# Kernel optimization log

Measured on AMD Instinct MI355X. Metric: run time of the kernel, lower is better.

## Reference

```python
import jax, jax.numpy as jnp
import numpy as np

D = 2048      # hidden dim
H = 16        # heads
BSZ = 4       # batch
L = 2048      # seq len
BASE_DT = 0.1


def setup_inputs() -> dict:
    key = jax.random.key(0)
    ks = jax.random.split(key, 9)
    s = 1.0 / np.sqrt(D)
    x = jax.random.normal(ks[0], (BSZ, L, D), dtype=jnp.float32)
    v = jax.random.normal(ks[1], (BSZ, L, D), dtype=jnp.float32)
    force = jax.random.normal(ks[2], (BSZ, L, D), dtype=jnp.float32)
    WA = jax.random.normal(ks[3], (D, D), dtype=jnp.float32) * s
    bA = jnp.zeros((D,), dtype=jnp.float32)
    WB = jax.random.normal(ks[4], (D, D), dtype=jnp.float32) * s
    bB = jnp.zeros((D,), dtype=jnp.float32)
    Wdt = jax.random.normal(ks[5], (D, D), dtype=jnp.float32) * s
    bdt = jnp.zeros((D,), dtype=jnp.float32)
    # base_dt_scales buffer: 1.5**head_index, repeated head_dim times
    scales = jnp.repeat(1.5 ** jnp.arange(H, dtype=jnp.float32), D // H)
    return {"x": x, "v": v, "force": force, "WA": WA, "bA": bA,
            "WB": WB, "bB": bB, "Wdt": Wdt, "bdt": bdt, "scales": scales}


def _combine(e1, e2):
    # associative op for v_t = a_t * v_{t-1} + b_t ; e1 is the earlier element
    a1, b1 = e1
    a2, b2 = e2
    return a1 * a2, a2 * b1 + b2


def reference(x, v, force, WA, bA, WB, bB, Wdt, bdt, scales):
    # x is LayerNorm-ed in the original but the result is unused; v is unused.
    A = jax.nn.sigmoid(force @ WA + bA)                      # [B, L, D] in (0,1)
    dt = jax.nn.softplus(force @ Wdt + bdt) * BASE_DT * scales  # per-head dt scaling
    B_val = (force @ WB + bB) * dt
    # parallel associative scan over the sequence axis: v_t = A_t v_{t-1} + B_t
    _, v_seq = jax.lax.associative_scan(_combine, (A, B_val), axis=1)
    # second scan has A=1 -> plain prefix sum
    x_seq = jnp.cumsum(v_seq * dt, axis=1)
    return x_seq, v_seq
```

## Files before the change

### kernel.cpp

```cpp
#include <hip/hip_runtime.h>
#include <hip/hip_bf16.h>
#include <cstdint>
#include <cstddef>

#define D_DIM 2048
#define L_SEQ 2048
#define B_SZ 4
#define M_ROWS (B_SZ * L_SEQ)
#define NT_COLS (3 * D_DIM)
#define NCH 16
#define CHUNK (L_SEQ / NCH)

typedef __bf16 bf16_t;
typedef bf16_t bf16x4 __attribute__((ext_vector_type(4)));
typedef bf16_t bf16x8 __attribute__((ext_vector_type(8)));
typedef float f32x4 __attribute__((ext_vector_type(4)));

__device__ __forceinline__ void gl_lds16(const void* g, void* l) {
    __builtin_amdgcn_global_load_lds(
        (const __attribute__((address_space(1))) unsigned int*)g,
        (__attribute__((address_space(3))) unsigned int*)l, 16, 0, 0);
}

__global__ __launch_bounds__(256) void cvt_bf16_kernel(
    const float* __restrict__ in, bf16_t* __restrict__ out, int n4)
{
    int i = blockIdx.x * 256 + threadIdx.x;
    if (i >= n4) return;
    float4 f = ((const float4*)in)[i];
    bf16x4 o;
    o[0] = (bf16_t)f.x; o[1] = (bf16_t)f.y; o[2] = (bf16_t)f.z; o[3] = (bf16_t)f.w;
    ((bf16x4*)out)[i] = o;
}

__global__ __launch_bounds__(256) void transpose_w_kernel(
    const float* __restrict__ W, bf16_t* __restrict__ Wt)
{
    __shared__ float tile[32][33];
    int j0 = blockIdx.x * 32, k0 = blockIdx.y * 32;
    int tx = threadIdx.x, ty = threadIdx.y;
#pragma unroll
    for (int i = 0; i < 4; i++) {
        int k = k0 + ty + i * 8;
        tile[ty + i * 8][tx] = W[(size_t)k * D_DIM + j0 + tx];
    }
    __syncthreads();
#pragma unroll
    for (int i = 0; i < 4; i++) {
        int j = j0 + ty + i * 8;
        Wt[(size_t)j * D_DIM + k0 + tx] = (bf16_t)tile[tx][ty + i * 8];
    }
}

__global__ __launch_bounds__(256) void gemm_fused_kernel(
    const bf16_t* __restrict__ Abf,
    const bf16_t* __restrict__ Wt,
    const float* __restrict__ bA, const float* __restrict__ bdt,
    const float* __restrict__ bB, const float* __restrict__ scales,
    float* __restrict__ outA,
    float* __restrict__ outDT,
    float* __restrict__ outB)
{
    __shared__ bf16_t lds_a[128 * 32];
    __shared__ bf16_t lds_b[128 * 32];

    const int bm0 = blockIdx.x * 128;
    const int bn0 = blockIdx.y * 128;
    const int t = threadIdx.x;
    const int lane = t & 63, w = t >> 6;
    const int wr = (w >> 1) * 64;
    const int wc = (w & 1) * 64;

    f32x4 acc[4][4] = {};

    const int lin0 = t, lin1 = t + 256;
    const int ar0 = lin0 >> 2, ac0 = (lin0 & 3) * 8;
    const int ar1 = lin1 >> 2, ac1 = (lin1 & 3) * 8;
    const int frow = lane & 15;
    const int fk = (lane >> 4) * 8;

    for (int k0 = 0; k0 < D_DIM; k0 += 32) {
        gl_lds16(Abf + (size_t)(bm0 + ar0) * D_DIM + k0 + ac0, lds_a + w * 512);
        gl_lds16(Abf + (size_t)(bm0 + ar1) * D_DIM + k0 + ac1, lds_a + 2048 + w * 512);
        gl_lds16(Wt  + (size_t)(bn0 + ar0) * D_DIM + k0 + ac0, lds_b + w * 512);
        gl_lds16(Wt  + (size_t)(bn0 + ar1) * D_DIM + k0 + ac1, lds_b + 2048 + w * 512);
        __syncthreads();

        bf16x8 af[4], bfr[4];
#pragma unroll
        for (int m = 0; m < 4; m++)
            af[m] = *(const bf16x8*)&lds_a[(wr + m * 16 + frow) * 32 + fk];
#pragma unroll
        for (int n = 0; n < 4; n++)
            bfr[n] = *(const bf16x8*)&lds_b[(wc + n * 16 + frow) * 32 + fk];
#pragma unroll
        for (int m = 0; m < 4; m++)
#pragma unroll
            for (int n = 0; n < 4; n++)
                acc[m][n] = __builtin_amdgcn_mfma_f32_16x16x32_bf16(
                    af[m], bfr[n], acc[m][n], 0, 0, 0);
        __syncthreads();
    }

    const int seg = bn0 >> 11;
    const int dbase = (bn0 & 2047) + wc + (lane & 15);
    const int rowbase = bm0 + wr + ((lane >> 4) << 2);
#pragma unroll
    for (int m = 0; m < 4; m++) {
#pragma unroll
        for (int n = 0; n < 4; n++) {
            int d = dbase + n * 16;
#pragma unroll
            for (int r = 0; r < 4; r++) {
                int gm = rowbase + m * 16 + r;
                size_t idx = (size_t)gm * D_DIM + d;
                float val = acc[m][n][r];
                if (seg == 0) {
                    outA[idx] = 1.0f / (1.0f + __expf(-(val + bA[d])));
                } else if (seg == 1) {
                    float xx = val + bdt[d];
                    float sp = xx > 0.f ? xx + log1pf(__expf(-xx)) : log1pf(__expf(xx));
                    outDT[idx] = sp * 0.1f * scales[d];
                } else {
                    outB[idx] = val + bB[d];
                }
            }
        }
    }
}

__global__ __launch_bounds__(256) void scan_pass1_kernel(
    const float* __restrict__ Aarr, const float* __restrict__ Braw,
    const float* __restrict__ dtarr, float4* __restrict__ agg)
{
    int tid = blockIdx.x * 256 + threadIdx.x;
    int d = tid & (D_DIM - 1);
    int c = (tid >> 11) & (NCH - 1);
    int b = tid >> 15;
    size_t base = ((size_t)b * L_SEQ + c * CHUNK) * D_DIM + d;
    float P = 1.f, R = 0.f, U = 0.f, Wg = 0.f;
#pragma unroll 4
    for (int tt = 0; tt < CHUNK; tt++) {
        size_t idx = base + (size_t)tt * D_DIM;
        float a = Aarr[idx], rb = Braw[idx], dt = dtarr[idx];
        float bv = rb * dt;
        float da = dt * a;
        R = da * P + R;
        Wg = da * U + dt * bv + Wg;
        U = a * U + bv;
        P = a * P;
    }
    agg[tid] = make_float4(P, R, U, Wg);
}

__global__ __launch_bounds__(256) void scan_pass2_kernel(
    const float4* __restrict__ agg, float2* __restrict__ pre)
{
    int tid = blockIdx.x * 256 + threadIdx.x;
    int d = tid & (D_DIM - 1);
    int b = tid >> 11;
    float v = 0.f, x = 0.f;
#pragma unroll
    for (int c = 0; c < NCH; c++) {
        int i = ((b * NCH + c) << 11) + d;
        float4 g = agg[i];
        pre[i] = make_float2(v, x);
        float vn = g.x * v + g.z;
        x = g.y * v + x + g.w;
        v = vn;
    }
}

__global__ __launch_bounds__(256) void scan_pass3_kernel(
    const float* __restrict__ dtarr, const float2* __restrict__ pre,
    float* __restrict__ xout ,
    float* __restrict__ vout )
{
    int tid = blockIdx.x * 256 + threadIdx.x;
    int d = tid & (D_DIM - 1);
    int c = (tid >> 11) & (NCH - 1);
    int b = tid >> 15;
    float2 s = pre[((b * NCH + c) << 11) + d];
    float v = s.x, x = s.y;
    size_t base = ((size_t)b * L_SEQ + c * CHUNK) * D_DIM + d;
#pragma unroll 4
    for (int tt = 0; tt < CHUNK; tt++) {
        size_t idx = base + (size_t)tt * D_DIM;
        float a = xout[idx];
        float rb = vout[idx];
        float dt = dtarr[idx];
        v = a * v + rb * dt;
        x = x + v * dt;
        vout[idx] = v;
        xout[idx] = x;
    }
}

extern "C" void kernel_launch(void* const* d_in, const int* in_sizes, int n_in,
                              void* d_out, int out_size, void* d_ws, size_t ws_size,
                              hipStream_t stream) {
    const float* force  = (const float*)d_in[2];
    const float* WA     = (const float*)d_in[3];
    const float* bA     = (const float*)d_in[4];
    const float* WB     = (const float*)d_in[5];
    const float* bB     = (const float*)d_in[6];
    const float* Wdt    = (const float*)d_in[7];
    const float* bdt    = (const float*)d_in[8];
    const float* scales = (const float*)d_in[9];

    float* xout = (float*)d_out;
    float* vout = xout + (size_t)M_ROWS * D_DIM;

    char* ws = (char*)d_ws;
    bf16_t* fbf = (bf16_t*)ws;
    bf16_t* wt  = (bf16_t*)(ws + (size_t)33554432);
    float*  dtv = (float*)(ws + (size_t)33554432 + 25165824);
    float4* agg = (float4*)(ws + (size_t)33554432 + 25165824 + 67108864);
    float2* pre = (float2*)(ws + (size_t)33554432 + 25165824 + 67108864 + 2097152);

    {
        int n4 = M_ROWS * D_DIM / 4;
        cvt_bf16_kernel<<<n4 / 256, 256, 0, stream>>>(force, fbf, n4);
    }
    {
        dim3 grid(D_DIM / 32, D_DIM / 32), block(32, 8);
        transpose_w_kernel<<<grid, block, 0, stream>>>(WA,  wt);
        transpose_w_kernel<<<grid, block, 0, stream>>>(Wdt, wt + (size_t)D_DIM * D_DIM);
        transpose_w_kernel<<<grid, block, 0, stream>>>(WB,  wt + (size_t)2 * D_DIM * D_DIM);
    }
    {
        dim3 grid(M_ROWS / 128, NT_COLS / 128);
        gemm_fused_kernel<<<grid, 256, 0, stream>>>(fbf, wt, bA, bdt, bB, scales,
                                                    xout, dtv, vout);
    }
    scan_pass1_kernel<<<(B_SZ * NCH * D_DIM) / 256, 256, 0, stream>>>(xout, vout, dtv, agg);
    scan_pass2_kernel<<<(B_SZ * D_DIM) / 256, 256, 0, stream>>>(agg, pre);
    scan_pass3_kernel<<<(B_SZ * NCH * D_DIM) / 256, 256, 0, stream>>>(dtv, pre, xout, vout);
}
```

Measured before the change: 498.6 us.

## Rewrite GEMM as 256x256 tile, 8-wave, double-buffered LDS pipeline with swizzle

Replaces the 128x128, single-buffered GEMM with a 256x256-tile kernel using 8 waves, a 128KB double-buffered LDS staging area filled asynchronously through global_load_lds, and XOR-swizzled LDS addressing. Loads for the next k-tiles are interleaved with MFMA groups using explicit vmcnt waits, raw barriers and setprio. Block IDs are remapped for better L2 locality. Bias loads are hoisted out of the epilogue. The aim is to raise MFMA utilization and cut per-k-step barrier stalls and LDS bank conflicts, at the cost of high register pressure and fragile manual synchronization.

After: 709.4 us. +42.3%, slower.

```diff
diff --git a/kernel.cpp b/kernel.cpp
--- a/kernel.cpp
+++ b/kernel.cpp
@@ -10,6 +10,7 @@
 #define NT_COLS (3 * D_DIM)
 #define NCH 16
 #define CHUNK (L_SEQ / NCH)
+#define KTILES (D_DIM / 64)
 
 typedef __bf16 bf16_t;
 typedef bf16_t bf16x4 __attribute__((ext_vector_type(4)));
@@ -21,6 +22,10 @@
         (const __attribute__((address_space(1))) unsigned int*)g,
         (__attribute__((address_space(3))) unsigned int*)l, 16, 0, 0);
 }
+
+#define BAR() asm volatile("s_barrier" ::: "memory")
+#define VMCNT4() asm volatile("s_waitcnt vmcnt(4)" ::: "memory")
+#define VMCNT0() asm volatile("s_waitcnt vmcnt(0)" ::: "memory")
 
 __global__ __launch_bounds__(256) void cvt_bf16_kernel(
     const float* __restrict__ in, bf16_t* __restrict__ out, int n4)
@@ -52,7 +57,39 @@
     }
 }
 
-__global__ __launch_bounds__(256) void gemm_fused_kernel(
+__device__ __forceinline__ void stage_half(const bf16_t* gp, int kofs,
+                                           char* ldsreg, int w, int lane)
+{
+    const int r0 = w * 32 + (lane >> 2);
+    const int gc = (((lane & 3) ^ ((lane >> 3) & 3)) << 3);
+    gl_lds16(gp + (size_t)r0 * D_DIM + kofs + gc, ldsreg + w * 2048);
+    gl_lds16(gp + (size_t)(r0 + 16) * D_DIM + kofs + gc, ldsreg + w * 2048 + 1024);
+}
+
+#define READ_FRAGS(BUF, KS, AF, BF) {                                          \
+    const char* ra_ = lds + (BUF) * 32768 + (KS) * 16384;                      \
+    const char* rb_ = ra_ + 65536;                                             \
+    _Pragma("unroll") for (int mm = 0; mm < 4; mm++)                           \
+        AF[mm] = *(const bf16x8*)(ra_ + ((wmBase + mm * 16) << 6) + loff);     \
+    _Pragma("unroll") for (int nn = 0; nn < 4; nn++)                           \
+        BF[nn] = *(const bf16x8*)(rb_ + ((wnBase + nn * 16) << 6) + loff);     \
+    _Pragma("unroll") for (int mm = 4; mm < 8; mm++)                           \
+        AF[mm] = *(const bf16x8*)(ra_ + ((wmBase + mm * 16) << 6) + loff); }
+
+#define MFMA_QUAD(MH, AF, BF)                                                  \
+    __builtin_amdgcn_s_setprio(1);                                             \
+    _Pragma("unroll") for (int mm = 0; mm < 4; mm++)                           \
+        _Pragma("unroll") for (int nn = 0; nn < 4; nn++)                       \
+            acc[(MH) * 4 + mm][nn] = __builtin_amdgcn_mfma_f32_16x16x32_bf16(  \
+                AF[(MH) * 4 + mm], BF[nn], acc[(MH) * 4 + mm][nn], 0, 0, 0);   \
+    __builtin_amdgcn_s_setprio(0);
+
+#define STAGE_A(BUF, T, KS) stage_half(gA, (T) * 64 + (KS) * 32,               \
+        lds + (BUF) * 32768 + (KS) * 16384, w, lane)
+#define STAGE_B(BUF, T, KS) stage_half(gB, (T) * 64 + (KS) * 32,               \
+        lds + 65536 + (BUF) * 32768 + (KS) * 16384, w, lane)
+
+__global__ __launch_bounds__(512, 2) void gemm_fused_kernel(
     const bf16_t* __restrict__ Abf,
     const bf16_t* __restrict__ Wt,
     const float* __restrict__ bA, const float* __restrict__ bdt,
@@ -61,71 +98,124 @@
     float* __restrict__ outDT,
     float* __restrict__ outB)
 {
-    __shared__ bf16_t lds_a[128 * 32];
-    __shared__ bf16_t lds_b[128 * 32];
-
-    const int bm0 = blockIdx.x * 128;
-    const int bn0 = blockIdx.y * 128;
-    const int t = threadIdx.x;
-    const int lane = t & 63, w = t >> 6;
-    const int wr = (w >> 1) * 64;
-    const int wc = (w & 1) * 64;
-
-    f32x4 acc[4][4] = {};
-
-    const int lin0 = t, lin1 = t + 256;
-    const int ar0 = lin0 >> 2, ac0 = (lin0 & 3) * 8;
-    const int ar1 = lin1 >> 2, ac1 = (lin1 & 3) * 8;
+    __shared__ __align__(1024) char lds[131072];
+
+    const int bid = blockIdx.x;
+    const int u = (bid & 7) * 96 + (bid >> 3);
+    const int bm0 = (u / 24) * 256;
+    const int bn0 = (u % 24) * 256;
+
+    const int tid = threadIdx.x;
+    const int lane = tid & 63;
+    const int w = tid >> 6;
+    const int wm = w >> 2;
+    const int wn = w & 3;
+    const int wmBase = wm * 128;
+    const int wnBase = wn * 64;
+
     const int frow = lane & 15;
-    const int fk = (lane >> 4) * 8;
-
-    for (int k0 = 0; k0 < D_DIM; k0 += 32) {
-        gl_lds16(Abf + (size_t)(bm0 + ar0) * D_DIM + k0 + ac0, lds_a + w * 512);
-        gl_lds16(Abf + (size_t)(bm0 + ar1) * D_DIM + k0 + ac1, lds_a + 2048 + w * 512);
-        gl_lds16(Wt  + (size_t)(bn0 + ar0) * D_DIM + k0 + ac0, lds_b + w * 512);
-        gl_lds16(Wt  + (size_t)(bn0 + ar1) * D_DIM + k0 + ac1, lds_b + 2048 + w * 512);
-        __syncthreads();
-
-        bf16x8 af[4], bfr[4];
-#pragma unroll
-        for (int m = 0; m < 4; m++)
-            af[m] = *(const bf16x8*)&lds_a[(wr + m * 16 + frow) * 32 + fk];
-#pragma unroll
-        for (int n = 0; n < 4; n++)
-            bfr[n] = *(const bf16x8*)&lds_b[(wc + n * 16 + frow) * 32 + fk];
-#pragma unroll
-        for (int m = 0; m < 4; m++)
+    const int loff = frow * 64 + (((lane >> 4) << 4) ^ (((frow >> 1) & 3) << 4));
+
+    const bf16_t* gA = Abf + (size_t)bm0 * D_DIM;
+    const bf16_t* gB = Wt + (size_t)bn0 * D_DIM;
+
+    f32x4 acc[8][4] = {};
+    bf16x8 af0[8], af1[8], bf0[4], bf1[4];
+
+    STAGE_A(0, 0, 0); STAGE_B(0, 0, 0); STAGE_A(0, 0, 1); STAGE_B(0, 0, 1);
+    STAGE_A(1, 1, 0); STAGE_B(1, 1, 0);
+    VMCNT4();
+    BAR();
+
+    for (int i = 0; i < KTILES / 2; ++i) {
+        const int t = 2 * i;
+        const bool nl = (i < KTILES / 2 - 1);
+
+        READ_FRAGS(0, 0, af0, bf0);
+        STAGE_A(1, t + 1, 1);
+        BAR();
+        MFMA_QUAD(0, af0, bf0);
+        BAR();
+        READ_FRAGS(0, 1, af1, bf1);
+        STAGE_B(1, t + 1, 1);
+        BAR();
+        MFMA_QUAD(1, af0, bf0);
+        BAR();
+        if (nl) STAGE_A(0, t + 2, 0);
+        BAR();
+        MFMA_QUAD(0, af1, bf1);
+        BAR();
+        if (nl) STAGE_B(0, t + 2, 0);
+        BAR();
+        MFMA_QUAD(1, af1, bf1);
+        if (nl) { VMCNT4(); } else { VMCNT0(); }
+        BAR();
+        READ_FRAGS(1, 0, af0, bf0);
+        if (nl) STAGE_A(0, t + 2, 1);
+        BAR();
+        MFMA_QUAD(0, af0, bf0);
+        BAR();
+        READ_FRAGS(1, 1, af1, bf1);
+        if (nl) STAGE_B(0, t + 2, 1);
+        BAR();
+        MFMA_QUAD(1, af0, bf0);
+        BAR();
+        if (nl) STAGE_A(1, t + 3, 0);
+        BAR();
+        MFMA_QUAD(0, af1, bf1);
+        BAR();
+        if (nl) STAGE_B(1, t + 3, 0);
+        BAR();
+        MFMA_QUAD(1, af1, bf1);
+        if (nl) { VMCNT4(); }
+        BAR();
+    }
+
+    const int seg = bn0 >> 11;
+    const int colb = (bn0 & 2047) + wnBase + (lane & 15);
+    const int rowb = bm0 + wmBase + ((lane >> 4) << 2);
+
+    if (seg == 0) {
+        float bias[4];
+#pragma unroll
+        for (int n = 0; n < 4; n++) bias[n] = bA[colb + n * 16];
+#pragma unroll
+        for (int m = 0; m < 8; m++)
 #pragma unroll
             for (int n = 0; n < 4; n++)
-                acc[m][n] = __builtin_amdgcn_mfma_f32_16x16x32_bf16(
-                    af[m], bfr[n], acc[m][n], 0, 0, 0);
-        __syncthreads();
-    }
-
-    const int seg = bn0 >> 11;
-    const int dbase = (bn0 & 2047) + wc + (lane & 15);
-    const int rowbase = bm0 + wr + ((lane >> 4) << 2);
-#pragma unroll
-    for (int m = 0; m < 4; m++) {
-#pragma unroll
-        for (int n = 0; n < 4; n++) {
-            int d = dbase + n * 16;
-#pragma unroll
-            for (int r = 0; r < 4; r++) {
-                int gm = rowbase + m * 16 + r;
-                size_t idx = (size_t)gm * D_DIM + d;
-                float val = acc[m][n][r];
-                if (seg == 0) {
-                    outA[idx] = 1.0f / (1.0f + __expf(-(val + bA[d])));
-                } else if (seg == 1) {
-                    float xx = val + bdt[d];
+#pragma unroll
+                for (int r = 0; r < 4; r++) {
+                    size_t idx = (size_t)(rowb + m * 16 + r) * D_DIM + colb + n * 16;
+                    outA[idx] = 1.0f / (1.0f + __expf(-(acc[m][n][r] + bias[n])));
+                }
+    } else if (seg == 1) {
+        float bias[4], sc[4];
+#pragma unroll
+        for (int n = 0; n < 4; n++) { bias[n] = bdt[colb + n * 16]; sc[n] = scales[colb + n * 16]; }
+#pragma unroll
+        for (int m = 0; m < 8; m++)
+#pragma unroll
+            for (int n = 0; n < 4; n++)
+#pragma unroll
+                for (int r = 0; r < 4; r++) {
+                    size_t idx = (size_t)(rowb + m * 16 + r) * D_DIM + colb + n * 16;
+                    float xx = acc[m][n][r] + bias[n];
                     float sp = xx > 0.f ? xx + log1pf(__expf(-xx)) : log1pf(__expf(xx));
-                    outDT[idx] = sp * 0.1f * scales[d];
-                } else {
-                    outB[idx] = val + bB[d];
+                    outDT[idx] = sp * 0.1f * sc[n];
                 }
-            }
-        }
+    } else {
+        float bias[4];
+#pragma unroll
+        for (int n = 0; n < 4; n++) bias[n] = bB[colb + n * 16];
+#pragma unroll
+        for (int m = 0; m < 8; m++)
+#pragma unroll
+            for (int n = 0; n < 4; n++)
+#pragma unroll
+                for (int r = 0; r < 4; r++) {
+                    size_t idx = (size_t)(rowb + m * 16 + r) * D_DIM + colb + n * 16;
+                    outB[idx] = acc[m][n][r] + bias[n];
+                }
     }
 }
 
@@ -173,8 +263,7 @@
 
 __global__ __launch_bounds__(256) void scan_pass3_kernel(
     const float* __restrict__ dtarr, const float2* __restrict__ pre,
-    float* __restrict__ xout ,
-    float* __restrict__ vout )
+    float* __restrict__ xout, float* __restrict__ vout)
 {
     int tid = blockIdx.x * 256 + threadIdx.x;
     int d = tid & (D_DIM - 1);
@@ -229,8 +318,8 @@
         transpose_w_kernel<<<grid, block, 0, stream>>>(WB,  wt + (size_t)2 * D_DIM * D_DIM);
     }
     {
-        dim3 grid(M_ROWS / 128, NT_COLS / 128);
-        gemm_fused_kernel<<<grid, 256, 0, stream>>>(fbf, wt, bA, bdt, bB, scales,
+        dim3 grid((M_ROWS / 256) * (NT_COLS / 256));
+        gemm_fused_kernel<<<grid, 512, 0, stream>>>(fbf, wt, bA, bdt, bB, scales,
                                                     xout, dtv, vout);
     }
     scan_pass1_kernel<<<(B_SZ * NCH * D_DIM) / 256, 256, 0, stream>>>(xout, vout, dtv, agg);
```
